# Optimization experiments

Hardware: AMD Instinct MI355X
Metric: run time of the kernel (lower is better)

## Reference

```python
import jax, jax.numpy as jnp
import numpy as np

D_MODEL = 1024
N_HEAD = 16


def setup_inputs() -> dict:
    key = jax.random.key(0)
    ks = jax.random.split(key, 11)
    B, T, D = 4, 2048, D_MODEL
    s = 1.0 / np.sqrt(D)
    inp = {
        "q": jax.random.normal(ks[0], (B, T, D), jnp.float32),
        "k": jax.random.normal(ks[1], (B, T, D), jnp.float32),
        "v": jax.random.normal(ks[2], (B, T, D), jnp.float32),
        "wq": jax.random.normal(ks[3], (D, D), jnp.float32) * s,
        "bq": jnp.zeros((D,), jnp.float32),
        "wk": jax.random.normal(ks[4], (D, D), jnp.float32) * s,
        "bk": jnp.zeros((D,), jnp.float32),
        "wv": jax.random.normal(ks[5], (D, D), jnp.float32) * s,
        "bv": jnp.zeros((D,), jnp.float32),
        "wo": jax.random.normal(ks[6], (D, D), jnp.float32) * s,
        "bo": jnp.zeros((D,), jnp.float32),
    }
    return inp


def reference(q, k, v, wq, bq, wk, bk, wv, bv, wo, bo):
    B, T, D = q.shape
    H = N_HEAD
    hd = D // H  # head dim
    # torch nn.Linear: y = x @ W.T + b
    qh = (q @ wq.T + bq).reshape(B, T, H, hd).transpose(0, 2, 1, 3)  # [B,H,T,hd]
    kh = (k @ wk.T + bk).reshape(B, T, H, hd).transpose(0, 2, 1, 3)
    vh = (v @ wv.T + bv).reshape(B, T, H, hd).transpose(0, 2, 1, 3)
    scale = 1.0 / jnp.sqrt(jnp.asarray(hd, qh.dtype))
    score = jnp.einsum("bhqd,bhkd->bhqk", qh, kh) * scale  # [B,H,T,T]
    causal = jnp.tril(jnp.ones((T, T), dtype=bool))
    score = jnp.where(causal, score, jnp.asarray(-jnp.inf, score.dtype))
    attn = jax.nn.softmax(score, axis=-1)
    out = jnp.einsum("bhqk,bhkd->bhqd", attn, vh)  # [B,H,T,hd]
    out = out.transpose(0, 2, 1, 3).reshape(B, T, D)
    return out @ wo.T + bo
```

## Files before the change

### kernel.cpp

```cpp
#include <hip/hip_runtime.h>
#include <hip/hip_bf16.h>

#define D_MODEL 1024
#define N_HEAD  16
#define HD      64
#define T_SEQ   2048
#define B_SZ    4
#define M_ROWS  (B_SZ * T_SEQ)

typedef __bf16 bf16;
typedef __bf16 bf16x4 __attribute__((ext_vector_type(4)));
typedef __bf16 bf16x8 __attribute__((ext_vector_type(8)));
typedef float  floatx4 __attribute__((ext_vector_type(4)));

__device__ __forceinline__ floatx4 fzero4() {
    floatx4 z = {0.f, 0.f, 0.f, 0.f};
    return z;
}

__device__ __forceinline__ void async_ld16(const void* g, void* l) {
    __builtin_amdgcn_global_load_lds(
        (const __attribute__((address_space(1))) void*)g,
        (__attribute__((address_space(3))) void*)l,
        16, 0, 0);
}

__global__ __launch_bounds__(256) void cvt4_kernel(
    const float* s0, bf16* d0, int n0,
    const float* s1, bf16* d1, int n1,
    const float* s2, bf16* d2, int n2,
    const float* s3, bf16* d3, int n3)
{
    const float* src; bf16* dst; int n8;
    switch (blockIdx.y) {
        case 0:  src = s0; dst = d0; n8 = n0; break;
        case 1:  src = s1; dst = d1; n8 = n1; break;
        case 2:  src = s2; dst = d2; n8 = n2; break;
        default: src = s3; dst = d3; n8 = n3; break;
    }
    int i = blockIdx.x * blockDim.x + threadIdx.x;
    int stride = gridDim.x * blockDim.x;
    for (; i < n8; i += stride) {
        float4 a = ((const float4*)src)[2 * i];
        float4 b = ((const float4*)src)[2 * i + 1];
        bf16x8 o;
        o[0] = (bf16)a.x; o[1] = (bf16)a.y; o[2] = (bf16)a.z; o[3] = (bf16)a.w;
        o[4] = (bf16)b.x; o[5] = (bf16)b.y; o[6] = (bf16)b.z; o[7] = (bf16)b.w;
        ((bf16x8*)dst)[i] = o;
    }
}

template <int OMODE>
__global__ __launch_bounds__(256) void gemm_bf16(
    const bf16* __restrict__ A0, const bf16* __restrict__ W0,
    const float* __restrict__ b0v, void* __restrict__ O0,
    const bf16* __restrict__ A1, const bf16* __restrict__ W1,
    const float* __restrict__ b1v, void* __restrict__ O1)
{
    __shared__ bf16 ldsA[128 * 64];
    __shared__ bf16 ldsW[128 * 64];

    const bf16* A    = blockIdx.z ? A1 : A0;
    const bf16* W    = blockIdx.z ? W1 : W0;
    const float* bias = blockIdx.z ? b1v : b0v;
    void* Out        = blockIdx.z ? O1 : O0;

    const int tid  = threadIdx.x;
    const int wave = tid >> 6, lane = tid & 63;
    const int quad = lane >> 4, l15 = lane & 15;
    const int wr = wave >> 1, wc = wave & 1;
    const int m0 = blockIdx.y * 128, n0 = blockIdx.x * 128;

    floatx4 acc[4][4];
#pragma unroll
    for (int i = 0; i < 4; ++i)
#pragma unroll
        for (int j = 0; j < 4; ++j) acc[i][j] = fzero4();

    const int ro = lane >> 3;
    const int gc = (lane & 7) ^ ro;
    const bf16* gA = A + (size_t)(m0 + wave * 32 + ro) * 1024 + gc * 8;
    const bf16* gW = W + (size_t)(n0 + wave * 32 + ro) * 1024 + gc * 8;

    for (int kt = 0; kt < 16; ++kt) {
        __syncthreads();
#pragma unroll
        for (int j = 0; j < 4; ++j)
            async_ld16((const void*)(gA + kt * 64 + j * 8 * 1024), &ldsA[(wave * 32 + j * 8) * 64]);
#pragma unroll
        for (int j = 0; j < 4; ++j)
            async_ld16((const void*)(gW + kt * 64 + j * 8 * 1024), &ldsW[(wave * 32 + j * 8) * 64]);
        __syncthreads();

#pragma unroll
        for (int ks = 0; ks < 2; ++ks) {
            const int pos = ((ks * 4 + quad) ^ (l15 & 7)) * 8;
            bf16x8 af[4], bw[4];
#pragma unroll
            for (int i = 0; i < 4; ++i)
                af[i] = *(const bf16x8*)(&ldsA[(wr * 64 + i * 16 + l15) * 64 + pos]);
#pragma unroll
            for (int j = 0; j < 4; ++j)
                bw[j] = *(const bf16x8*)(&ldsW[(wc * 64 + j * 16 + l15) * 64 + pos]);
#pragma unroll
            for (int i = 0; i < 4; ++i)
#pragma unroll
                for (int j = 0; j < 4; ++j)
                    acc[i][j] = __builtin_amdgcn_mfma_f32_16x16x32_bf16(af[i], bw[j], acc[i][j], 0, 0, 0);
        }
    }

#pragma unroll
    for (int i = 0; i < 4; ++i) {
#pragma unroll
        for (int j = 0; j < 4; ++j) {
#pragma unroll
            for (int r = 0; r < 4; ++r) {
                int m = m0 + wr * 64 + i * 16 + quad * 4 + r;
                int n = n0 + wc * 64 + j * 16 + l15;
                float val = acc[i][j][r] + bias[n];
                if (OMODE == 2) {
                    ((float*)Out)[(size_t)m * 1024 + n] = val;
                } else {
                    int b = m >> 11, t = m & 2047;
                    int h = n >> 6,  d = n & 63;
                    size_t addr;
                    if (OMODE == 0)
                        addr = ((size_t)(b * N_HEAD + h) * T_SEQ + t) * HD + d;
                    else
                        addr = ((size_t)(b * N_HEAD + h) * HD + d) * T_SEQ + t;
                    ((bf16*)Out)[addr] = (bf16)val;
                }
            }
        }
    }
}

__global__ __launch_bounds__(256, 3) void attn_kernel(
    const bf16* __restrict__ Qh, const bf16* __restrict__ Kh,
    const bf16* __restrict__ Vt, bf16* __restrict__ AO)
{
    __shared__ bf16 Ks[128 * 64];
    __shared__ bf16 Vts[64 * 128];
    __shared__ bf16 Ps[128 * 72];

    const int tid  = threadIdx.x;
    const int wave = tid >> 6, lane = tid & 63;
    const int quad = lane >> 4, l15 = lane & 15;
    const int qt = 15 - blockIdx.x, bh = blockIdx.y;
    const size_t base = (size_t)bh * T_SEQ * HD;

    bf16x8 qf[2][2];
    const bf16* qbase = Qh + base + (size_t)(qt * 128 + wave * 32) * HD;
#pragma unroll
    for (int ti = 0; ti < 2; ++ti)
#pragma unroll
        for (int ks = 0; ks < 2; ++ks)
            qf[ti][ks] = *(const bf16x8*)(qbase + (ti * 16 + l15) * HD + ks * 32 + quad * 8);

    const float scale2 = 0.125f * 1.44269504088896340736f;
    float mrow[2] = {-1e30f, -1e30f}, lrow[2] = {0.f, 0.f};
    floatx4 oacc[2][4];
#pragma unroll
    for (int ti = 0; ti < 2; ++ti)
#pragma unroll
        for (int nj = 0; nj < 4; ++nj) oacc[ti][nj] = fzero4();

    const int kro = lane >> 3;
    const int kgc = (lane & 7) ^ kro;
    const bf16* kg = Kh + base + (size_t)(wave * 32 + kro) * HD + kgc * 8;
    const int vrow_lo = (lane >> 4);
    const int vchunk  = (lane & 15);

    for (int kt = 0; kt <= qt; ++kt) {
        __syncthreads();
#pragma unroll
        for (int j = 0; j < 4; ++j)
            async_ld16((const void*)(kg + (size_t)(kt * 128 + j * 8) * HD),
                       &Ks[(wave * 32 + j * 8) * 64]);
#pragma unroll
        for (int j = 0; j < 4; ++j) {
            int d = wave * 16 + j * 4 + vrow_lo;
            int gcv = vchunk ^ (d & 15);
            async_ld16((const void*)(Vt + base + (size_t)d * T_SEQ + kt * 128 + gcv * 8),
                       &Vts[(wave * 16 + j * 4) * 128]);
        }
        __syncthreads();

        const bool diag = (kt == qt);
        const int lim = diag ? (2 * wave + 1) : 7;

        floatx4 sacc[2][8];
#pragma unroll
        for (int ti = 0; ti < 2; ++ti)
#pragma unroll
            for (int tj = 0; tj < 8; ++tj) sacc[ti][tj] = fzero4();
#pragma unroll
        for (int ks = 0; ks < 2; ++ks) {
            const int pos = ((ks * 4 + quad) ^ (l15 & 7)) * 8;
#pragma unroll
            for (int tj = 0; tj < 8; ++tj) {
                if (tj <= lim) {
                    bf16x8 kf = *(const bf16x8*)(&Ks[(tj * 16 + l15) * 64 + pos]);
                    sacc[0][tj] = __builtin_amdgcn_mfma_f32_16x16x32_bf16(kf, qf[0][ks], sacc[0][tj], 0, 0, 0);
                    sacc[1][tj] = __builtin_amdgcn_mfma_f32_16x16x32_bf16(kf, qf[1][ks], sacc[1][tj], 0, 0, 0);
                }
            }
        }

#pragma unroll
        for (int ti = 0; ti < 2; ++ti) {
            const int ql = wave * 32 + ti * 16 + l15;
            float mx = -1e30f;
#pragma unroll
            for (int tj = 0; tj < 8; ++tj) {
                if (tj <= lim) {
#pragma unroll
                    for (int r = 0; r < 4; ++r) {
                        float s = sacc[ti][tj][r] * scale2;
                        if (diag && (tj * 16 + quad * 4 + r) > ql) s = -1e30f;
                        sacc[ti][tj][r] = s;
                        mx = fmaxf(mx, s);
                    }
                }
            }
            mx = fmaxf(mx, __shfl_xor(mx, 16));
            mx = fmaxf(mx, __shfl_xor(mx, 32));
            float mnew  = fmaxf(mrow[ti], mx);
            float alpha = exp2f(mrow[ti] - mnew);
            float rsum  = 0.f;
#pragma unroll
            for (int tj = 0; tj < 8; ++tj) {
                if (tj <= lim) {
#pragma unroll
                    for (int r = 0; r < 4; ++r) {
                        float p = exp2f(sacc[ti][tj][r] - mnew);
                        rsum += p;
                        sacc[ti][tj][r] = p;
                    }
                }
            }
            rsum += __shfl_xor(rsum, 16);
            rsum += __shfl_xor(rsum, 32);
            lrow[ti] = lrow[ti] * alpha + rsum;
            mrow[ti] = mnew;
#pragma unroll
            for (int r = 0; r < 4; ++r) {
                float ar = __shfl(alpha, quad * 4 + r);
#pragma unroll
                for (int nj = 0; nj < 4; ++nj)
                    oacc[ti][nj][r] *= ar;
            }
        }

#pragma unroll
        for (int h = 0; h < 2; ++h) {
            if (4 * h > lim) break;
#pragma unroll
            for (int ti = 0; ti < 2; ++ti) {
                const int ql = wave * 32 + ti * 16 + l15;
#pragma unroll
                for (int tjo = 0; tjo < 4; ++tjo) {
                    int tj = 4 * h + tjo;
                    if (tj <= lim) {
                        bf16x4 pv;
#pragma unroll
                        for (int r = 0; r < 4; ++r) pv[r] = (bf16)sacc[ti][tj][r];
                        *(bf16x4*)(&Ps[ql * 72 + tjo * 16 + quad * 4]) = pv;
                    }
                }
            }
#pragma unroll
            for (int ks2 = 0; ks2 < 2; ++ks2) {
                const int gks = 2 * h + ks2;
                if (diag && gks > wave) break;
                bf16x8 pf[2];
                pf[0] = *(const bf16x8*)(&Ps[(wave * 32 + l15) * 72 + ks2 * 32 + quad * 8]);
                pf[1] = *(const bf16x8*)(&Ps[(wave * 32 + 16 + l15) * 72 + ks2 * 32 + quad * 8]);
#pragma unroll
                for (int nj = 0; nj < 4; ++nj) {
                    int pos = ((gks * 4 + quad) ^ l15) * 8;
                    bf16x8 vf = *(const bf16x8*)(&Vts[(nj * 16 + l15) * 128 + pos]);
                    oacc[0][nj] = __builtin_amdgcn_mfma_f32_16x16x32_bf16(pf[0], vf, oacc[0][nj], 0, 0, 0);
                    oacc[1][nj] = __builtin_amdgcn_mfma_f32_16x16x32_bf16(pf[1], vf, oacc[1][nj], 0, 0, 0);
                }
            }
        }
    }

    const int b = bh >> 4, h = bh & 15;
#pragma unroll
    for (int ti = 0; ti < 2; ++ti) {
#pragma unroll
        for (int r = 0; r < 4; ++r) {
            float lv = __shfl(lrow[ti], quad * 4 + r);
            float rl = 1.f / lv;
            int qrow = qt * 128 + wave * 32 + ti * 16 + quad * 4 + r;
#pragma unroll
            for (int nj = 0; nj < 4; ++nj) {
                int d = nj * 16 + l15;
                AO[((size_t)(b * T_SEQ + qrow)) * D_MODEL + h * HD + d] =
                    (bf16)(oacc[ti][nj][r] * rl);
            }
        }
    }
}

extern "C" void kernel_launch(void* const* d_in, const int* in_sizes, int n_in,
                              void* d_out, int out_size, void* d_ws, size_t ws_size,
                              hipStream_t stream)
{
    const float* q  = (const float*)d_in[0];
    const float* k  = (const float*)d_in[1];
    const float* v  = (const float*)d_in[2];
    const float* wq = (const float*)d_in[3];
    const float* bq = (const float*)d_in[4];
    const float* wk = (const float*)d_in[5];
    const float* bk = (const float*)d_in[6];
    const float* wv = (const float*)d_in[7];
    const float* bv = (const float*)d_in[8];
    const float* wo = (const float*)d_in[9];
    const float* bo = (const float*)d_in[10];

    char* ws  = (char*)d_ws;
    char* dob = (char*)d_out;
    const size_t SZ  = (size_t)M_ROWS * D_MODEL * sizeof(bf16);
    const size_t WSZ = (size_t)D_MODEL * D_MODEL * sizeof(bf16);

    bf16* Qb  = (bf16*)(dob);
    bf16* Kb  = (bf16*)(dob + SZ);
    bf16* Wvb = (bf16*)(dob);
    bf16* Wqb = (bf16*)(ws);
    bf16* Wkb = (bf16*)(ws + WSZ);
    bf16* Vb  = (bf16*)(ws);
    bf16* AO  = (bf16*)(ws);
    bf16* Qh  = (bf16*)(ws + SZ);
    bf16* Wob = (bf16*)(ws + SZ);
    bf16* Kh  = (bf16*)(ws + 2 * SZ);
    bf16* Vt  = (bf16*)(ws + 3 * SZ);

    const int NQ8 = M_ROWS * D_MODEL / 8;
    const int NW8 = D_MODEL * D_MODEL / 8;
    dim3 cb(256);
    dim3 gb(256);

    hipLaunchKernelGGL(cvt4_kernel, dim3(1024, 4), cb, 0, stream,
                       q, Qb, NQ8,  k, Kb, NQ8,  wq, Wqb, NW8,  wk, Wkb, NW8);
    hipLaunchKernelGGL((gemm_bf16<0>), dim3(8, 64, 2), gb, 0, stream,
                       Qb, Wqb, bq, (void*)Qh,  Kb, Wkb, bk, (void*)Kh);
    hipLaunchKernelGGL(cvt4_kernel, dim3(1024, 2), cb, 0, stream,
                       v, Vb, NQ8,  wv, Wvb, NW8,  (const float*)0, (bf16*)0, 0,
                       (const float*)0, (bf16*)0, 0);
    hipLaunchKernelGGL((gemm_bf16<1>), dim3(8, 64, 1), gb, 0, stream,
                       Vb, Wvb, bv, (void*)Vt,  Vb, Wvb, bv, (void*)Vt);
    hipLaunchKernelGGL(attn_kernel, dim3(16, 64), gb, 0, stream, Qh, Kh, Vt, AO);
    hipLaunchKernelGGL(cvt4_kernel, dim3(1024, 1), cb, 0, stream,
                       wo, Wob, NW8,  (const float*)0, (bf16*)0, 0,
                       (const float*)0, (bf16*)0, 0,  (const float*)0, (bf16*)0, 0);
    hipLaunchKernelGGL((gemm_bf16<2>), dim3(8, 64, 1), gb, 0, stream,
                       AO, Wob, bo, d_out,  AO, Wob, bo, d_out);
}
```

Baseline: 420.3 us.

## Merge conversions, fold softmax scale into Q projection, pair causal attention tiles

All seven fp32-to-bf16 conversions now run in one launch, replacing three separate cvt launches, and the workspace buffers are laid out again to fit. The softmax scale times log2(e) is applied in the Q projection epilogue, which removes a multiply per score in attention. The attention kernel moves to 512-thread blocks over 256-row query tiles. Each block handles a short and a long causal strip, (7-pair) and pair, to balance work across blocks and to use each loaded K/V tile for more query rows. The per-wave masking and skip logic is generalised to match, and Q is now rounded to bf16 after scaling.

Measured after the change: 602.5 us. 1.43x slower.

```diff
diff --git a/kernel.cpp b/kernel.cpp
--- a/kernel.cpp
+++ b/kernel.cpp
@@ -25,27 +25,25 @@
         16, 0, 0);
 }
 
-__global__ __launch_bounds__(256) void cvt4_kernel(
-    const float* s0, bf16* d0, int n0,
-    const float* s1, bf16* d1, int n1,
-    const float* s2, bf16* d2, int n2,
-    const float* s3, bf16* d3, int n3)
+struct CvtArgs {
+    const float* s[7];
+    bf16* d[7];
+    int n[7];
+};
+
+__global__ __launch_bounds__(256) void cvt7_kernel(CvtArgs a)
 {
-    const float* src; bf16* dst; int n8;
-    switch (blockIdx.y) {
-        case 0:  src = s0; dst = d0; n8 = n0; break;
-        case 1:  src = s1; dst = d1; n8 = n1; break;
-        case 2:  src = s2; dst = d2; n8 = n2; break;
-        default: src = s3; dst = d3; n8 = n3; break;
-    }
+    const float* src = a.s[blockIdx.y];
+    bf16* dst = a.d[blockIdx.y];
+    int n8 = a.n[blockIdx.y];
     int i = blockIdx.x * blockDim.x + threadIdx.x;
     int stride = gridDim.x * blockDim.x;
     for (; i < n8; i += stride) {
-        float4 a = ((const float4*)src)[2 * i];
-        float4 b = ((const float4*)src)[2 * i + 1];
+        float4 x = ((const float4*)src)[2 * i];
+        float4 y = ((const float4*)src)[2 * i + 1];
         bf16x8 o;
-        o[0] = (bf16)a.x; o[1] = (bf16)a.y; o[2] = (bf16)a.z; o[3] = (bf16)a.w;
-        o[4] = (bf16)b.x; o[5] = (bf16)b.y; o[6] = (bf16)b.z; o[7] = (bf16)b.w;
+        o[0] = (bf16)x.x; o[1] = (bf16)x.y; o[2] = (bf16)x.z; o[3] = (bf16)x.w;
+        o[4] = (bf16)y.x; o[5] = (bf16)y.y; o[6] = (bf16)y.z; o[7] = (bf16)y.w;
         ((bf16x8*)dst)[i] = o;
     }
 }
@@ -53,17 +51,18 @@
 template <int OMODE>
 __global__ __launch_bounds__(256) void gemm_bf16(
     const bf16* __restrict__ A0, const bf16* __restrict__ W0,
-    const float* __restrict__ b0v, void* __restrict__ O0,
+    const float* __restrict__ b0v, void* __restrict__ O0, float scl0,
     const bf16* __restrict__ A1, const bf16* __restrict__ W1,
-    const float* __restrict__ b1v, void* __restrict__ O1)
+    const float* __restrict__ b1v, void* __restrict__ O1, float scl1)
 {
     __shared__ bf16 ldsA[128 * 64];
     __shared__ bf16 ldsW[128 * 64];
 
-    const bf16* A    = blockIdx.z ? A1 : A0;
-    const bf16* W    = blockIdx.z ? W1 : W0;
+    const bf16* A     = blockIdx.z ? A1 : A0;
+    const bf16* W     = blockIdx.z ? W1 : W0;
     const float* bias = blockIdx.z ? b1v : b0v;
-    void* Out        = blockIdx.z ? O1 : O0;
+    void* Out         = blockIdx.z ? O1 : O0;
+    const float scl   = blockIdx.z ? scl1 : scl0;
 
     const int tid  = threadIdx.x;
     const int wave = tid >> 6, lane = tid & 63;
@@ -118,7 +117,7 @@
             for (int r = 0; r < 4; ++r) {
                 int m = m0 + wr * 64 + i * 16 + quad * 4 + r;
                 int n = n0 + wc * 64 + j * 16 + l15;
-                float val = acc[i][j][r] + bias[n];
+                float val = (acc[i][j][r] + bias[n]) * scl;
                 if (OMODE == 2) {
                     ((float*)Out)[(size_t)m * 1024 + n] = val;
                 } else {
@@ -136,171 +135,177 @@
     }
 }
 
-__global__ __launch_bounds__(256, 3) void attn_kernel(
+__global__ __launch_bounds__(512, 4) void attn_kernel(
     const bf16* __restrict__ Qh, const bf16* __restrict__ Kh,
     const bf16* __restrict__ Vt, bf16* __restrict__ AO)
 {
     __shared__ bf16 Ks[128 * 64];
     __shared__ bf16 Vts[64 * 128];
-    __shared__ bf16 Ps[128 * 72];
+    __shared__ bf16 Ps[256 * 72];
 
     const int tid  = threadIdx.x;
     const int wave = tid >> 6, lane = tid & 63;
     const int quad = lane >> 4, l15 = lane & 15;
-    const int qt = 15 - blockIdx.x, bh = blockIdx.y;
+    const int pair = blockIdx.x, bh = blockIdx.y;
     const size_t base = (size_t)bh * T_SEQ * HD;
-
-    bf16x8 qf[2][2];
-    const bf16* qbase = Qh + base + (size_t)(qt * 128 + wave * 32) * HD;
-#pragma unroll
-    for (int ti = 0; ti < 2; ++ti)
-#pragma unroll
-        for (int ks = 0; ks < 2; ++ks)
-            qf[ti][ks] = *(const bf16x8*)(qbase + (ti * 16 + l15) * HD + ks * 32 + quad * 8);
-
-    const float scale2 = 0.125f * 1.44269504088896340736f;
-    float mrow[2] = {-1e30f, -1e30f}, lrow[2] = {0.f, 0.f};
-    floatx4 oacc[2][4];
-#pragma unroll
-    for (int ti = 0; ti < 2; ++ti)
-#pragma unroll
-        for (int nj = 0; nj < 4; ++nj) oacc[ti][nj] = fzero4();
+    const int bb = bh >> 4, hh = bh & 15;
 
     const int kro = lane >> 3;
     const int kgc = (lane & 7) ^ kro;
-    const bf16* kg = Kh + base + (size_t)(wave * 32 + kro) * HD + kgc * 8;
-    const int vrow_lo = (lane >> 4);
-    const int vchunk  = (lane & 15);
-
-    for (int kt = 0; kt <= qt; ++kt) {
-        __syncthreads();
-#pragma unroll
-        for (int j = 0; j < 4; ++j)
-            async_ld16((const void*)(kg + (size_t)(kt * 128 + j * 8) * HD),
-                       &Ks[(wave * 32 + j * 8) * 64]);
-#pragma unroll
-        for (int j = 0; j < 4; ++j) {
-            int d = wave * 16 + j * 4 + vrow_lo;
-            int gcv = vchunk ^ (d & 15);
-            async_ld16((const void*)(Vt + base + (size_t)d * T_SEQ + kt * 128 + gcv * 8),
-                       &Vts[(wave * 16 + j * 4) * 128]);
+
+    for (int phase = 0; phase < 2; ++phase) {
+        const int st = phase ? pair : 7 - pair;
+        const int ktmax = 2 * st + 1;
+        const int qb = st * 256 + wave * 32;
+
+        bf16x8 qf[2][2];
+        const bf16* qbase = Qh + base + (size_t)qb * HD;
+#pragma unroll
+        for (int ti = 0; ti < 2; ++ti)
+#pragma unroll
+            for (int ks = 0; ks < 2; ++ks)
+                qf[ti][ks] = *(const bf16x8*)(qbase + (ti * 16 + l15) * HD + ks * 32 + quad * 8);
+
+        float mrow[2] = {-1e30f, -1e30f}, lrow[2] = {0.f, 0.f};
+        floatx4 oacc[2][4];
+#pragma unroll
+        for (int ti = 0; ti < 2; ++ti)
+#pragma unroll
+            for (int nj = 0; nj < 4; ++nj) oacc[ti][nj] = fzero4();
+
+        for (int kt = 0; kt <= ktmax; ++kt) {
+            __syncthreads();
+#pragma unroll
+            for (int j = 0; j < 2; ++j)
+                async_ld16((const void*)(Kh + base +
+                               (size_t)(kt * 128 + wave * 16 + j * 8 + kro) * HD + kgc * 8),
+                           &Ks[(wave * 16 + j * 8) * 64]);
+#pragma unroll
+            for (int j = 0; j < 2; ++j) {
+                int d = wave * 8 + j * 4 + (lane >> 4);
+                int gcv = (lane & 15) ^ (d & 15);
+                async_ld16((const void*)(Vt + base + (size_t)d * T_SEQ + kt * 128 + gcv * 8),
+                           &Vts[(wave * 8 + j * 4) * 128]);
+            }
+            __syncthreads();
+
+            const int limr = qb + 31 - kt * 128;
+            if (limr < 0) continue;
+            const int gksmax = limr >= 96 ? 3 : (limr >> 5);
+            const int lim = 2 * gksmax + 1;
+            const bool msk = (qb < kt * 128 + 127);
+
+            floatx4 sacc[2][8];
+#pragma unroll
+            for (int ti = 0; ti < 2; ++ti)
+#pragma unroll
+                for (int tj = 0; tj < 8; ++tj) sacc[ti][tj] = fzero4();
+#pragma unroll
+            for (int ks = 0; ks < 2; ++ks) {
+                const int pos = ((ks * 4 + quad) ^ (l15 & 7)) * 8;
+#pragma unroll
+                for (int tj = 0; tj < 8; ++tj) {
+                    if (tj <= lim) {
+                        bf16x8 kf = *(const bf16x8*)(&Ks[(tj * 16 + l15) * 64 + pos]);
+                        sacc[0][tj] = __builtin_amdgcn_mfma_f32_16x16x32_bf16(kf, qf[0][ks], sacc[0][tj], 0, 0, 0);
+                        sacc[1][tj] = __builtin_amdgcn_mfma_f32_16x16x32_bf16(kf, qf[1][ks], sacc[1][tj], 0, 0, 0);
+                    }
+                }
+            }
+
+#pragma unroll
+            for (int ti = 0; ti < 2; ++ti) {
+                const int qg = qb + ti * 16 + l15;
+                float mx = -1e30f;
+#pragma unroll
+                for (int tj = 0; tj < 8; ++tj) {
+                    if (tj <= lim) {
+#pragma unroll
+                        for (int r = 0; r < 4; ++r) {
+                            float s = sacc[ti][tj][r];
+                            if (msk && (kt * 128 + tj * 16 + quad * 4 + r) > qg) s = -1e30f;
+                            sacc[ti][tj][r] = s;
+                            mx = fmaxf(mx, s);
+                        }
+                    }
+                }
+                mx = fmaxf(mx, __shfl_xor(mx, 16));
+                mx = fmaxf(mx, __shfl_xor(mx, 32));
+                float mnew  = fmaxf(mrow[ti], mx);
+                float alpha = exp2f(mrow[ti] - mnew);
+                float rsum  = 0.f;
+#pragma unroll
+                for (int tj = 0; tj < 8; ++tj) {
+                    if (tj <= lim) {
+#pragma unroll
+                        for (int r = 0; r < 4; ++r) {
+                            float p = exp2f(sacc[ti][tj][r] - mnew);
+                            rsum += p;
+                            sacc[ti][tj][r] = p;
+                        }
+                    }
+                }
+                rsum += __shfl_xor(rsum, 16);
+                rsum += __shfl_xor(rsum, 32);
+                lrow[ti] = lrow[ti] * alpha + rsum;
+                mrow[ti] = mnew;
+#pragma unroll
+                for (int r = 0; r < 4; ++r) {
+                    float ar = __shfl(alpha, quad * 4 + r);
+#pragma unroll
+                    for (int nj = 0; nj < 4; ++nj)
+                        oacc[ti][nj][r] *= ar;
+                }
+            }
+
+#pragma unroll
+            for (int h2 = 0; h2 < 2; ++h2) {
+                if (4 * h2 > lim) break;
+#pragma unroll
+                for (int ti = 0; ti < 2; ++ti) {
+                    const int ql = wave * 32 + ti * 16 + l15;
+#pragma unroll
+                    for (int tjo = 0; tjo < 4; ++tjo) {
+                        int tj = 4 * h2 + tjo;
+                        if (tj <= lim) {
+                            bf16x4 pv;
+#pragma unroll
+                            for (int r = 0; r < 4; ++r) pv[r] = (bf16)sacc[ti][tj][r];
+                            *(bf16x4*)(&Ps[ql * 72 + tjo * 16 + quad * 4]) = pv;
+                        }
+                    }
+                }
+#pragma unroll
+                for (int ks2 = 0; ks2 < 2; ++ks2) {
+                    const int gks = 2 * h2 + ks2;
+                    if (gks > gksmax) break;
+                    bf16x8 pf[2];
+                    pf[0] = *(const bf16x8*)(&Ps[(wave * 32 + l15) * 72 + ks2 * 32 + quad * 8]);
+                    pf[1] = *(const bf16x8*)(&Ps[(wave * 32 + 16 + l15) * 72 + ks2 * 32 + quad * 8]);
+#pragma unroll
+                    for (int nj = 0; nj < 4; ++nj) {
+                        int pos = ((gks * 4 + quad) ^ l15) * 8;
+                        bf16x8 vf = *(const bf16x8*)(&Vts[(nj * 16 + l15) * 128 + pos]);
+                        oacc[0][nj] = __builtin_amdgcn_mfma_f32_16x16x32_bf16(pf[0], vf, oacc[0][nj], 0, 0, 0);
+                        oacc[1][nj] = __builtin_amdgcn_mfma_f32_16x16x32_bf16(pf[1], vf, oacc[1][nj], 0, 0, 0);
+                    }
+                }
+            }
         }
-        __syncthreads();
-
-        const bool diag = (kt == qt);
-        const int lim = diag ? (2 * wave + 1) : 7;
-
-        floatx4 sacc[2][8];
-#pragma unroll
-        for (int ti = 0; ti < 2; ++ti)
-#pragma unroll
-            for (int tj = 0; tj < 8; ++tj) sacc[ti][tj] = fzero4();
-#pragma unroll
-        for (int ks = 0; ks < 2; ++ks) {
-            const int pos = ((ks * 4 + quad) ^ (l15 & 7)) * 8;
-#pragma unroll
-            for (int tj = 0; tj < 8; ++tj) {
-                if (tj <= lim) {
-                    bf16x8 kf = *(const bf16x8*)(&Ks[(tj * 16 + l15) * 64 + pos]);
-                    sacc[0][tj] = __builtin_amdgcn_mfma_f32_16x16x32_bf16(kf, qf[0][ks], sacc[0][tj], 0, 0, 0);
-                    sacc[1][tj] = __builtin_amdgcn_mfma_f32_16x16x32_bf16(kf, qf[1][ks], sacc[1][tj], 0, 0, 0);
-                }
-            }
-        }
 
 #pragma unroll
         for (int ti = 0; ti < 2; ++ti) {
-            const int ql = wave * 32 + ti * 16 + l15;
-            float mx = -1e30f;
-#pragma unroll
-            for (int tj = 0; tj < 8; ++tj) {
-                if (tj <= lim) {
-#pragma unroll
-                    for (int r = 0; r < 4; ++r) {
-                        float s = sacc[ti][tj][r] * scale2;
-                        if (diag && (tj * 16 + quad * 4 + r) > ql) s = -1e30f;
-                        sacc[ti][tj][r] = s;
-                        mx = fmaxf(mx, s);
-                    }
-                }
-            }
-            mx = fmaxf(mx, __shfl_xor(mx, 16));
-            mx = fmaxf(mx, __shfl_xor(mx, 32));
-            float mnew  = fmaxf(mrow[ti], mx);
-            float alpha = exp2f(mrow[ti] - mnew);
-            float rsum  = 0.f;
-#pragma unroll
-            for (int tj = 0; tj < 8; ++tj) {
-                if (tj <= lim) {
-#pragma unroll
-                    for (int r = 0; r < 4; ++r) {
-                        float p = exp2f(sacc[ti][tj][r] - mnew);
-                        rsum += p;
-                        sacc[ti][tj][r] = p;
-                    }
-                }
-            }
-            rsum += __shfl_xor(rsum, 16);
-            rsum += __shfl_xor(rsum, 32);
-            lrow[ti] = lrow[ti] * alpha + rsum;
-            mrow[ti] = mnew;
 #pragma unroll
             for (int r = 0; r < 4; ++r) {
-                float ar = __shfl(alpha, quad * 4 + r);
-#pragma unroll
-                for (int nj = 0; nj < 4; ++nj)
-                    oacc[ti][nj][r] *= ar;
-            }
-        }
-
-#pragma unroll
-        for (int h = 0; h < 2; ++h) {
-            if (4 * h > lim) break;
-#pragma unroll
-            for (int ti = 0; ti < 2; ++ti) {
-                const int ql = wave * 32 + ti * 16 + l15;
-#pragma unroll
-                for (int tjo = 0; tjo < 4; ++tjo) {
-                    int tj = 4 * h + tjo;
-                    if (tj <= lim) {
-                        bf16x4 pv;
-#pragma unroll
-                        for (int r = 0; r < 4; ++r) pv[r] = (bf16)sacc[ti][tj][r];
-                        *(bf16x4*)(&Ps[ql * 72 + tjo * 16 + quad * 4]) = pv;
-                    }
-                }
-            }
-#pragma unroll
-            for (int ks2 = 0; ks2 < 2; ++ks2) {
-                const int gks = 2 * h + ks2;
-                if (diag && gks > wave) break;
-                bf16x8 pf[2];
-                pf[0] = *(const bf16x8*)(&Ps[(wave * 32 + l15) * 72 + ks2 * 32 + quad * 8]);
-                pf[1] = *(const bf16x8*)(&Ps[(wave * 32 + 16 + l15) * 72 + ks2 * 32 + quad * 8]);
+                float lv = __shfl(lrow[ti], quad * 4 + r);
+                float rl = 1.f / lv;
+                int qrow = qb + ti * 16 + quad * 4 + r;
 #pragma unroll
                 for (int nj = 0; nj < 4; ++nj) {
-                    int pos = ((gks * 4 + quad) ^ l15) * 8;
-                    bf16x8 vf = *(const bf16x8*)(&Vts[(nj * 16 + l15) * 128 + pos]);
-                    oacc[0][nj] = __builtin_amdgcn_mfma_f32_16x16x32_bf16(pf[0], vf, oacc[0][nj], 0, 0, 0);
-                    oacc[1][nj] = __builtin_amdgcn_mfma_f32_16x16x32_bf16(pf[1], vf, oacc[1][nj], 0, 0, 0);
-                }
-            }
-        }
-    }
-
-    const int b = bh >> 4, h = bh & 15;
-#pragma unroll
-    for (int ti = 0; ti < 2; ++ti) {
-#pragma unroll
-        for (int r = 0; r < 4; ++r) {
-            float lv = __shfl(lrow[ti], quad * 4 + r);
-            float rl = 1.f / lv;
-            int qrow = qt * 128 + wave * 32 + ti * 16 + quad * 4 + r;
-#pragma unroll
-            for (int nj = 0; nj < 4; ++nj) {
-                int d = nj * 16 + l15;
-                AO[((size_t)(b * T_SEQ + qrow)) * D_MODEL + h * HD + d] =
-                    (bf16)(oacc[ti][nj][r] * rl);
+                    int d = nj * 16 + l15;
+                    AO[((size_t)(bb * T_SEQ + qrow)) * D_MODEL + hh * HD + d] =
+                        (bf16)(oacc[ti][nj][r] * rl);
+                }
             }
         }
     }
@@ -324,39 +329,42 @@
 
     char* ws  = (char*)d_ws;
     char* dob = (char*)d_out;
-    const size_t SZ  = (size_t)M_ROWS * D_MODEL * sizeof(bf16);
-    const size_t WSZ = (size_t)D_MODEL * D_MODEL * sizeof(bf16);
-
+    const size_t MB = 1024 * 1024;
+
+    bf16* Wqb = (bf16*)(ws);
+    bf16* Wkb = (bf16*)(ws + 2 * MB);
+    bf16* Wvb = (bf16*)(ws + 4 * MB);
+    bf16* Vb  = (bf16*)(ws + 6 * MB);
+    bf16* AO  = (bf16*)(ws + 6 * MB);
+    bf16* Qh  = (bf16*)(ws + 22 * MB);
+    bf16* Kh  = (bf16*)(ws + 38 * MB);
+    bf16* Wob = (bf16*)(ws + 54 * MB);
     bf16* Qb  = (bf16*)(dob);
-    bf16* Kb  = (bf16*)(dob + SZ);
-    bf16* Wvb = (bf16*)(dob);
-    bf16* Wqb = (bf16*)(ws);
-    bf16* Wkb = (bf16*)(ws + WSZ);
-    bf16* Vb  = (bf16*)(ws);
-    bf16* AO  = (bf16*)(ws);
-    bf16* Qh  = (bf16*)(ws + SZ);
-    bf16* Wob = (bf16*)(ws + SZ);
-    bf16* Kh  = (bf16*)(ws + 2 * SZ);
-    bf16* Vt  = (bf16*)(ws + 3 * SZ);
+    bf16* Kb  = (bf16*)(dob + 16 * MB);
+    bf16* Vt  = (bf16*)(dob);
 
     const int NQ8 = M_ROWS * D_MODEL / 8;
     const int NW8 = D_MODEL * D_MODEL / 8;
-    dim3 cb(256);
-    dim3 gb(256);
-
-    hipLaunchKernelGGL(cvt4_kernel, dim3(1024, 4), cb, 0, stream,
-                       q, Qb, NQ8,  k, Kb, NQ8,  wq, Wqb, NW8,  wk, Wkb, NW8);
-    hipLaunchKernelGGL((gemm_bf16<0>), dim3(8, 64, 2), gb, 0, stream,
-                       Qb, Wqb, bq, (void*)Qh,  Kb, Wkb, bk, (void*)Kh);
-    hipLaunchKernelGGL(cvt4_kernel, dim3(1024, 2), cb, 0, stream,
-                       v, Vb, NQ8,  wv, Wvb, NW8,  (const float*)0, (bf16*)0, 0,
-                       (const float*)0, (bf16*)0, 0);
-    hipLaunchKernelGGL((gemm_bf16<1>), dim3(8, 64, 1), gb, 0, stream,
-                       Vb, Wvb, bv, (void*)Vt,  Vb, Wvb, bv, (void*)Vt);
-    hipLaunchKernelGGL(attn_kernel, dim3(16, 64), gb, 0, stream, Qh, Kh, Vt, AO);
-    hipLaunchKernelGGL(cvt4_kernel, dim3(1024, 1), cb, 0, stream,
-                       wo, Wob, NW8,  (const float*)0, (bf16*)0, 0,
-                       (const float*)0, (bf16*)0, 0,  (const float*)0, (bf16*)0, 0);
-    hipLaunchKernelGGL((gemm_bf16<2>), dim3(8, 64, 1), gb, 0, stream,
-                       AO, Wob, bo, d_out,  AO, Wob, bo, d_out);
-}
+    const float QSCALE = 0.18033688011112042f;
+
+    CvtArgs ca;
+    ca.s[0] = q;  ca.d[0] = Qb;  ca.n[0] = NQ8;
+    ca.s[1] = k;  ca.d[1] = Kb;  ca.n[1] = NQ8;
+    ca.s[2] = v;  ca.d[2] = Vb;  ca.n[2] = NQ8;
+    ca.s[3] = wq; ca.d[3] = Wqb; ca.n[3] = NW8;
+    ca.s[4] = wk; ca.d[4] = Wkb; ca.n[4] = NW8;
+    ca.s[5] = wv; ca.d[5] = Wvb; ca.n[5] = NW8;
+    ca.s[6] = wo; ca.d[6] = Wob; ca.n[6] = NW8;
+
+    hipLaunchKernelGGL(cvt7_kernel, dim3(512, 7), dim3(256), 0, stream, ca);
+    hipLaunchKernelGGL((gemm_bf16<0>), dim3(8, 64, 2), dim3(256), 0, stream,
+                       Qb, Wqb, bq, (void*)Qh, QSCALE,
+                       Kb, Wkb, bk, (void*)Kh, 1.0f);
+    hipLaunchKernelGGL((gemm_bf16<1>), dim3(8, 64, 1), dim3(256), 0, stream,
+                       Vb, Wvb, bv, (void*)Vt, 1.0f,
+                       Vb, Wvb, bv, (void*)Vt, 1.0f);
+    hipLaunchKernelGGL(attn_kernel, dim3(4, 64), dim3(512), 0, stream, Qh, Kh, Vt, AO);
+    hipLaunchKernelGGL((gemm_bf16<2>), dim3(8, 64, 1), dim3(256), 0, stream,
+                       AO, Wob, bo, d_out, 1.0f,
+                       AO, Wob, bo, d_out, 1.0f);
+}
```
